# Optimization experiments

Measured on AMD Instinct MI355X. Metric: run time of the kernel, lower is better.

## Reference

```python
import jax, jax.numpy as jnp
import numpy as np
from jax import lax

B, H, W = 2, 256, 256
K = 7
K2 = K * K
IN_CH = 32 * 2 + 81  # 145


def _conv(x, w, b):
    y = lax.conv_general_dilated(x, w, (1, 1), 'SAME', dimension_numbers=('NCHW', 'OIHW', 'NCHW'))
    return y + b[None, :, None, None]


def _lrelu(x):
    return jnp.where(x >= 0, x, 0.1 * x)


def _predictor(x, w1, b1, w2, b2, w3, b3, wo, bo, ww, bw):
    f = _lrelu(_conv(x, w1, b1))
    f = _lrelu(_conv(f, w2, b2))
    f = _lrelu(_conv(f, w3, b3))
    offsets = _conv(f, wo, bo)                     # (B, 2*K2, H, W)
    weights = jax.nn.softmax(_conv(f, ww, bw), 1)  # (B, K2, H, W)
    return offsets, weights


def _sample(image, offsets, weights):
    b, c, h, w = image.shape
    k2 = weights.shape[1]
    off = offsets.reshape(b, k2, 2, h, w)
    dx, dy = off[:, :, 0], off[:, :, 1]
    gy, gx = jnp.meshgrid(jnp.arange(h, dtype=image.dtype), jnp.arange(w, dtype=image.dtype), indexing='ij')
    sx = gx[None, None] + dx  # (b,k2,h,w)
    sy = gy[None, None] + dy
    # Original normalizes with 2*s/(n-1)-1 (align_corners=True formula) but calls
    # grid_sample(align_corners=False): pixel coord = ((g+1)*n - 1)/2 = s*n/(n-1) - 0.5.
    # padding_mode='border' == clamp coord to [0, n-1] before bilinear.
    px = jnp.clip(sx * (w / (w - 1.0)) - 0.5, 0.0, w - 1.0)
    py = jnp.clip(sy * (h / (h - 1.0)) - 0.5, 0.0, h - 1.0)
    x0 = jnp.floor(px)
    y0 = jnp.floor(py)
    fx = (px - x0)[:, None]  # (b,1,k2,h,w)
    fy = (py - y0)[:, None]
    x0i = x0.astype(jnp.int32)
    y0i = y0.astype(jnp.int32)
    x1i = jnp.minimum(x0i + 1, w - 1)
    y1i = jnp.minimum(y0i + 1, h - 1)
    img = image.reshape(b, c, h * w)

    def gather(yi, xi):
        idx = (yi * w + xi).reshape(b, 1, k2 * h * w)
        return jnp.take_along_axis(img, idx, axis=2).reshape(b, c, k2, h, w)

    v00 = gather(y0i, x0i)
    v01 = gather(y0i, x1i)
    v10 = gather(y1i, x0i)
    v11 = gather(y1i, x1i)
    sampled = (v00 * (1 - fx) * (1 - fy) + v01 * fx * (1 - fy)
               + v10 * (1 - fx) * fy + v11 * fx * fy)
    return jnp.einsum('bkhw,bckhw->bchw', weights, sampled)


def setup_inputs() -> dict:
    key = jax.random.key(0)
    ks = iter(jax.random.split(key, 64))

    def nrm(shape, s=1.0):
        return jax.random.normal(next(ks), shape, jnp.float32) * s

    off0 = np.array([[j - K // 2, i - K // 2] for i in range(K) for j in range(K)],
                    np.float32).reshape(-1)  # interleaved (dx, dy) default grid

    def pred_params(p):
        return {
            p + '_w1': nrm((256, IN_CH, 3, 3), 0.02), p + '_b1': jnp.zeros((256,), jnp.float32),
            p + '_w2': nrm((256, 256, 3, 3), 0.02), p + '_b2': jnp.zeros((256,), jnp.float32),
            p + '_w3': nrm((128, 256, 3, 3), 0.02), p + '_b3': jnp.zeros((128,), jnp.float32),
            p + '_wo': nrm((2 * K2, 128, 3, 3), 0.01), p + '_bo': jnp.asarray(off0),
            p + '_ww': nrm((K2, 128, 3, 3), 0.02), p + '_bw': jnp.full((K2,), 1.0 / K2, jnp.float32),
        }

    inp = {
        'frame1': nrm((B, 3, H, W)),
        'frame2': nrm((B, 3, H, W)),
        'feat1': nrm((B, 32, H, W)),
        'feat2': nrm((B, 32, H, W)),
        'corr': nrm((B, 81, H, W)),
    }
    inp.update(pred_params('k1'))
    inp.update(pred_params('k2'))
    inp['bl_w1'] = nrm((64, IN_CH, 3, 3), 0.02)
    inp['bl_b1'] = jnp.zeros((64,), jnp.float32)
    inp['bl_w2'] = nrm((1, 64, 3, 3), 0.02)
    inp['bl_b2'] = jnp.zeros((1,), jnp.float32)
    return inp


def reference(frame1, frame2, feat1, feat2, corr,
              k1_w1, k1_b1, k1_w2, k1_b2, k1_w3, k1_b3, k1_wo, k1_bo, k1_ww, k1_bw,
              k2_w1, k2_b1, k2_w2, k2_b2, k2_w3, k2_b3, k2_wo, k2_bo, k2_ww, k2_bw,
              bl_w1, bl_b1, bl_w2, bl_b2):
    combined = jnp.concatenate([feat1, feat2, corr], axis=1)  # (B,145,H,W)
    off1, wt1 = _predictor(combined, k1_w1, k1_b1, k1_w2, k1_b2, k1_w3, k1_b3, k1_wo, k1_bo, k1_ww, k1_bw)
    off2, wt2 = _predictor(combined, k2_w1, k2_b1, k2_w2, k2_b2, k2_w3, k2_b3, k2_wo, k2_bo, k2_ww, k2_bw)
    s1 = _sample(frame1, off1, wt1)
    s2 = _sample(frame2, off2, wt2)
    blend = jax.nn.sigmoid(_conv(_lrelu(_conv(combined, bl_w1, bl_b1)), bl_w2, bl_b2))
    output = blend * s1 + (1.0 - blend) * s2
    return (output, blend, off1, off2, wt1, wt2)
```

## Files before the change

kernel.cpp:

```cpp
#include <hip/hip_runtime.h>


static constexpr int HW  = 65536;
static constexpr int WID = 256;
static constexpr int PAD = 66564;

using f32x16 = __attribute__((ext_vector_type(16))) float;
using f32x4  = __attribute__((ext_vector_type(4))) float;
using s16x8  = __attribute__((ext_vector_type(8))) short;

__device__ __forceinline__ unsigned short f2b(float f) {
    unsigned u = __builtin_bit_cast(unsigned, f);
    u += 0x7fffu + ((u >> 16) & 1u);
    return (unsigned short)(u >> 16);
}
__device__ __forceinline__ float b2f(unsigned short h) {
    unsigned u = ((unsigned)h) << 16;
    return __builtin_bit_cast(float, u);
}

template <int N> __device__ __forceinline__ void vm_wait() {
    asm volatile("s_waitcnt vmcnt(%0)" :: "n"(N) : "memory");
}

__global__ void pack_x(const float* __restrict__ feat1, const float* __restrict__ feat2,
                       const float* __restrict__ corr, unsigned short* __restrict__ Xc) {
    int idx = blockIdx.x * 256 + threadIdx.x;
    int g  = idx >> 17;
    int bp = idx & (2 * HW - 1);
    int b  = bp >> 16, p = bp & 65535;
    unsigned short v[8];
#pragma unroll
    for (int j = 0; j < 8; ++j) {
        int c = g * 8 + j;
        float val = 0.f;
        if (c < 32)       val = feat1[(size_t)(b * 32 + c) * HW + p];
        else if (c < 64)  val = feat2[(size_t)(b * 32 + (c - 32)) * HW + p];
        else if (c < 145) val = corr [(size_t)(b * 81 + (c - 64)) * HW + p];
        v[j] = f2b(val);
    }
    uint4 u;
    u.x = v[0] | ((unsigned)v[1] << 16);
    u.y = v[2] | ((unsigned)v[3] << 16);
    u.z = v[4] | ((unsigned)v[5] << 16);
    u.w = v[6] | ((unsigned)v[7] << 16);
    int y = p >> 8, x = p & 255;
    size_t cell = (size_t)b * PAD + (size_t)(y + 1) * 258 + (x + 1);
    *reinterpret_cast<uint4*>(Xc + cell * 160 + g * 8) = u;
}

__global__ void pack_w(const float* __restrict__ W, unsigned short* __restrict__ Wp,
                       int OC, int IC, int OCP, int KC) {
    int idx = blockIdx.x * 256 + threadIdx.x;
    int total = 9 * KC * 4 * OCP * 8;
    if (idx >= total) return;
    int i8 = idx & 7;  int r = idx >> 3;
    int oc = r % OCP;  r /= OCP;
    int g  = r & 3;    r >>= 2;
    int kb = r % KC;   int s = r / KC;
    int ic = kb * 32 + g * 8 + i8;
    float v = (oc < OC && ic < IC) ? W[((size_t)(oc * IC + ic)) * 9 + s] : 0.f;
    Wp[idx] = f2b(v);
}

__global__ void zero_border(unsigned short* __restrict__ buf, int C) {
    int idx = blockIdx.x * 256 + threadIdx.x;
    int G = C >> 3;
    int total = 2 * 1028 * G;
    if (idx >= total) return;
    int gi = idx % G; int r = idx / G;
    int ci = r % 1028; int b = r / 1028;
    int row, col;
    if (ci < 258)      { row = 0;            col = ci; }
    else if (ci < 516) { row = 257;          col = ci - 258; }
    else if (ci < 772) { row = ci - 516 + 1; col = 0; }
    else               { row = ci - 772 + 1; col = 257; }
    *reinterpret_cast<uint4*>(buf + ((size_t)b * PAD + row * 258 + col) * C + gi * 8) =
        make_uint4(0u, 0u, 0u, 0u);
}

template <int ICP, int OCF, int OCT, int MODE>
__global__ __launch_bounds__(512, 2) void conv3x3(
    const unsigned short* __restrict__ X,
    const uint4* __restrict__ Wp,
    const float* __restrict__ bias,
    unsigned short* __restrict__ outB,
    float* __restrict__ outF)
{
    constexpr int KC = ICP / 32;
    __shared__ uint4 lds[8192];

    const int t = threadIdx.x;
    const int lane = t & 63, wn = t >> 6;
    const int l31 = lane & 31, hi = lane >> 5;
    const int ocOff = blockIdx.y * 128;

    const int bid = blockIdx.x;
    const int q8  = gridDim.x >> 3;
    const int work = (bid & 7) * q8 + (bid >> 3);
    const int bb = work >> 7;
    const int tt = work & 127;
    const int tr = tt >> 3, tc = tt & 7;

    auto stage_x = [&](int kb2, int slot) {
#pragma unroll
        for (int it = 0; it < 5; ++it) {
            int G = it * 512 + t;
            int g = G / 640;
            int cell = G - g * 640;
            cell = min(cell, 611);
            int rr = cell / 34, cc = cell - rr * 34;
            const unsigned short* src = X +
                ((size_t)bb * PAD + (size_t)(tr * 16 + rr) * 258 + tc * 32 + cc) * ICP +
                kb2 * 32 + g * 8;
            __builtin_amdgcn_global_load_lds(
                (const __attribute__((address_space(1))) unsigned int*)src,
                (__attribute__((address_space(3))) unsigned int*)&lds[slot * 2560 + it * 512 + (t & ~63)],
                16, 0, 0);
        }
    };
    auto stage_wg = [&](int kb2, int dy2, int wslot) {
#pragma unroll
        for (int j = 0; j < 3; ++j) {
            int s = dy2 * 3 + j;
            const uint4* src = Wp + ((size_t)(s * KC + kb2) * 4 + (t >> 7)) * OCF + ocOff + (t & 127);
            __builtin_amdgcn_global_load_lds(
                (const __attribute__((address_space(1))) unsigned int*)src,
                (__attribute__((address_space(3))) unsigned int*)&lds[5120 + wslot * 1536 + j * 512 + (t & ~63)],
                16, 0, 0);
        }
    };

    f32x16 acc[4][2] = {};

    stage_x(0, 0);
    stage_wg(0, 0, 0);

#pragma unroll 1
    for (int kb = 0; kb < KC; ++kb) {
        const int xb = (kb & 1) * 2560;
#pragma unroll
        for (int dy = 0; dy < 3; ++dy) {
            const int wb = 5120 + ((kb * 3 + dy) & 1) * 1536;
            __builtin_amdgcn_s_barrier();
            const bool lastG = (kb == KC - 1) && (dy == 2);
            if (dy == 0) {
                stage_wg(kb, 1, (kb * 3 + 1) & 1);
            } else if (dy == 1) {
                stage_wg(kb, 2, (kb * 3 + 2) & 1);
            } else if (kb + 1 < KC) {
                stage_wg(kb + 1, 0, (3 * (kb + 1)) & 1);
                stage_x(kb + 1, (kb + 1) & 1);
            }
            if (lastG)        vm_wait<0>();
            else if (dy == 2) vm_wait<8>();
            else              vm_wait<3>();

#pragma unroll
            for (int dxi = 0; dxi < 3; ++dxi) {
                uint4 a[2][4], bq[2][2];
#pragma unroll
                for (int ks = 0; ks < 2; ++ks) {
#pragma unroll
                    for (int fm = 0; fm < 4; ++fm)
                        a[ks][fm] = lds[wb + dxi * 512 + (ks * 2 + hi) * 128 + fm * 32 + l31];
#pragma unroll
                    for (int fn = 0; fn < 2; ++fn)
                        bq[ks][fn] = lds[xb + (ks * 2 + hi) * 640 + (wn * 2 + fn + dy) * 34 + dxi + l31];
                }
                __builtin_amdgcn_s_setprio(1);
#pragma unroll
                for (int ks = 0; ks < 2; ++ks)
#pragma unroll
                    for (int fm = 0; fm < 4; ++fm)
#pragma unroll
                        for (int fn = 0; fn < 2; ++fn)
                            acc[fm][fn] = __builtin_amdgcn_mfma_f32_32x32x16_bf16(
                                __builtin_bit_cast(s16x8, a[ks][fm]),
                                __builtin_bit_cast(s16x8, bq[ks][fn]),
                                acc[fm][fn], 0, 0, 0);
                __builtin_amdgcn_s_setprio(0);
            }
        }
    }

#pragma unroll
    for (int fm = 0; fm < 4; ++fm) {
#pragma unroll
        for (int fn = 0; fn < 2; ++fn) {
            const int prow = wn * 2 + fn;
            if (MODE == 0) {
                const size_t cellp = (size_t)bb * PAD + (size_t)(tr * 16 + prow + 1) * 258 + tc * 32 + l31 + 1;
#pragma unroll
                for (int qd = 0; qd < 4; ++qd) {
                    const int goc = ocOff + fm * 32 + qd * 8 + hi * 4;
                    if (goc < OCT) {
                        float4 bv = *reinterpret_cast<const float4*>(bias + goc);
                        const float* bvp = reinterpret_cast<const float*>(&bv);
                        unsigned short o[4];
#pragma unroll
                        for (int j = 0; j < 4; ++j) {
                            float r = acc[fm][fn][qd * 4 + j] + bvp[j];
                            r = (r >= 0.f) ? r : 0.1f * r;
                            o[j] = f2b(r);
                        }
                        uint2 pk;
                        pk.x = o[0] | ((unsigned)o[1] << 16);
                        pk.y = o[2] | ((unsigned)o[3] << 16);
                        *reinterpret_cast<uint2*>(outB + cellp * OCT + goc) = pk;
                    }
                }
            } else {
                const int py = tr * 16 + prow, px = tc * 32 + l31;
#pragma unroll
                for (int qd = 0; qd < 4; ++qd) {
#pragma unroll
                    for (int j = 0; j < 4; ++j) {
                        const int oc = ocOff + fm * 32 + qd * 8 + hi * 4 + j;
                        if (oc < OCT)
                            outF[((size_t)bb * OCT + oc) * HW + py * WID + px] =
                                acc[fm][fn][qd * 4 + j] + bias[oc];
                    }
                }
            }
        }
    }
}

__global__ void softmax49(float* __restrict__ L) {
    int idx = blockIdx.x * 256 + threadIdx.x;
    int b = idx >> 16, p = idx & 65535;
    float* lp = L + (size_t)b * 49 * HW + p;
    float v[49];
    float mx = -1e30f;
#pragma unroll
    for (int k = 0; k < 49; ++k) { v[k] = lp[(size_t)k * HW]; mx = fmaxf(mx, v[k]); }
    float sum = 0.f;
#pragma unroll
    for (int k = 0; k < 49; ++k) { v[k] = expf(v[k] - mx); sum += v[k]; }
    float inv = 1.f / sum;
#pragma unroll
    for (int k = 0; k < 49; ++k) lp[(size_t)k * HW] = v[k] * inv;
}

__global__ void blend2k(const unsigned short* __restrict__ Fb, const float* __restrict__ W2,
                        const float* __restrict__ B2, float* __restrict__ blendOut) {
    int idx = blockIdx.x * 256 + threadIdx.x;
    int b = idx >> 16, p = idx & 65535, y = p >> 8, x = p & 255;
    float acc = B2[0];
#pragma unroll
    for (int ry = 0; ry < 3; ++ry) {
#pragma unroll
        for (int rx = 0; rx < 3; ++rx) {
            const unsigned short* fp = Fb + ((size_t)b * PAD + (size_t)(y + ry) * 258 + (x + rx)) * 64;
#pragma unroll
            for (int g = 0; g < 8; ++g) {
                uint4 u = *reinterpret_cast<const uint4*>(fp + g * 8);
                unsigned w[4] = {u.x, u.y, u.z, u.w};
#pragma unroll
                for (int h = 0; h < 4; ++h) {
                    int c = g * 8 + h * 2;
                    acc += b2f((unsigned short)(w[h] & 0xffffu)) * W2[(c)     * 9 + ry * 3 + rx];
                    acc += b2f((unsigned short)(w[h] >> 16))     * W2[(c + 1) * 9 + ry * 3 + rx];
                }
            }
        }
    }
    blendOut[idx] = 1.f / (1.f + expf(-acc));
}

__global__ void pack_frames(const float* __restrict__ f1, const float* __restrict__ f2,
                            f32x4* __restrict__ Ff) {
    int idx = blockIdx.x * 256 + threadIdx.x;
    int fr = idx >> 17; int bp = idx & (2 * HW - 1);
    const float* src = fr ? f2 : f1;
    int b = bp >> 16, p = bp & 65535;
    f32x4 v;
    v[0] = src[(size_t)(b * 3 + 0) * HW + p];
    v[1] = src[(size_t)(b * 3 + 1) * HW + p];
    v[2] = src[(size_t)(b * 3 + 2) * HW + p];
    v[3] = 0.f;
    Ff[(size_t)fr * 2 * HW + bp] = v;
}

__device__ __forceinline__ void sample_accum4(const f32x4* __restrict__ img,
                                              const float* __restrict__ off,
                                              const float* __restrict__ wt,
                                              int x, int y, f32x4& s) {
    for (int k = 0; k < 49; ++k) {
        float dx = off[(size_t)(2 * k) * HW];
        float dy = off[(size_t)(2 * k + 1) * HW];
        float w  = wt [(size_t)k * HW];
        float px = ((float)x + dx) * (256.f / 255.f) - 0.5f;
        float py = ((float)y + dy) * (256.f / 255.f) - 0.5f;
        px = fminf(fmaxf(px, 0.f), 255.f);
        py = fminf(fmaxf(py, 0.f), 255.f);
        float x0f = floorf(px), y0f = floorf(py);
        float fx = px - x0f, fy = py - y0f;
        int x0 = (int)x0f, y0 = (int)y0f;
        int x1 = min(x0 + 1, 255), y1 = min(y0 + 1, 255);
        const f32x4* r0 = img + y0 * WID;
        const f32x4* r1 = img + y1 * WID;
        f32x4 v = (1.f - fy) * ((1.f - fx) * r0[x0] + fx * r0[x1]) +
                  fy         * ((1.f - fx) * r1[x0] + fx * r1[x1]);
        s += w * v;
    }
}

__global__ void sample_final(const f32x4* __restrict__ Ff,
                             const float* __restrict__ off1, const float* __restrict__ off2,
                             const float* __restrict__ wt1, const float* __restrict__ wt2,
                             const float* __restrict__ blend, float* __restrict__ out) {
    int idx = blockIdx.x * 256 + threadIdx.x;
    int b = idx >> 16, p = idx & 65535, y = p >> 8, x = p & 255;
    f32x4 s1 = {0.f, 0.f, 0.f, 0.f}, s2 = {0.f, 0.f, 0.f, 0.f};
    sample_accum4(Ff + (size_t)b * HW, off1 + (size_t)b * 98 * HW + p,
                  wt1 + (size_t)b * 49 * HW + p, x, y, s1);
    sample_accum4(Ff + (size_t)(2 + b) * HW, off2 + (size_t)b * 98 * HW + p,
                  wt2 + (size_t)b * 49 * HW + p, x, y, s2);
    float bl = blend[idx];
#pragma unroll
    for (int c = 0; c < 3; ++c)
        out[(size_t)(b * 3 + c) * HW + p] = bl * s1[c] + (1.f - bl) * s2[c];
}

extern "C" void kernel_launch(void* const* d_in, const int* in_sizes, int n_in,
                              void* d_out, int out_size, void* d_ws, size_t ws_size,
                              hipStream_t stream) {
    (void)in_sizes; (void)n_in; (void)out_size; (void)ws_size;
    const float* frame1 = (const float*)d_in[0];
    const float* frame2 = (const float*)d_in[1];
    const float* feat1  = (const float*)d_in[2];
    const float* feat2  = (const float*)d_in[3];
    const float* corr   = (const float*)d_in[4];
    const float* Wsrc[2][5];
    const float* Bsrc[2][5];
    for (int pdx = 0; pdx < 2; ++pdx) {
        int base = 5 + pdx * 10;
        for (int l = 0; l < 5; ++l) {
            Wsrc[pdx][l] = (const float*)d_in[base + 2 * l];
            Bsrc[pdx][l] = (const float*)d_in[base + 2 * l + 1];
        }
    }
    const float* bl_w1 = (const float*)d_in[25];
    const float* bl_b1 = (const float*)d_in[26];
    const float* bl_w2 = (const float*)d_in[27];
    const float* bl_b2 = (const float*)d_in[28];

    float* out      = (float*)d_out;
    float* out_bl   = out + 393216;
    float* out_off[2] = {out + 524288,   out + 13369344};
    float* out_wt [2] = {out + 26214400, out + 32636928};

    char* ws = (char*)d_ws;
    size_t o = 0;
    auto alloc = [&](size_t bytes) { char* p = ws + o; o += (bytes + 255) & ~(size_t)255; return p; };
    unsigned short* Xc   = (unsigned short*)alloc((size_t)2 * PAD * 160 * 2);
    unsigned short* bufA = (unsigned short*)alloc((size_t)2 * PAD * 256 * 2);
    unsigned short* bufB = (unsigned short*)alloc((size_t)2 * PAD * 256 * 2);
    unsigned short *WpC1[2], *WpC2[2], *WpC3[2], *WpCo[2], *WpCw[2];
    for (int pdx = 0; pdx < 2; ++pdx) {
        WpC1[pdx] = (unsigned short*)alloc((size_t)9 * 256 * 160 * 2);
        WpC2[pdx] = (unsigned short*)alloc((size_t)9 * 256 * 256 * 2);
        WpC3[pdx] = (unsigned short*)alloc((size_t)9 * 128 * 256 * 2);
        WpCo[pdx] = (unsigned short*)alloc((size_t)9 * 128 * 128 * 2);
        WpCw[pdx] = (unsigned short*)alloc((size_t)9 * 128 * 128 * 2);
    }
    unsigned short* WpBl = (unsigned short*)alloc((size_t)9 * 128 * 160 * 2);
    f32x4* Ff = (f32x4*)bufA;

    auto packw = [&](const float* W, unsigned short* Wp, int OC, int IC, int OCP, int ICP) {
        int total = 9 * OCP * ICP;
        pack_w<<<(total + 255) / 256, 256, 0, stream>>>(W, Wp, OC, IC, OCP, ICP / 32);
    };
    auto zb = [&](unsigned short* buf, int C) {
        int total = 2 * 1028 * (C / 8);
        zero_border<<<(total + 255) / 256, 256, 0, stream>>>(buf, C);
    };

    zb(Xc, 160);
    pack_x<<<(2 * HW * 20) / 256, 256, 0, stream>>>(feat1, feat2, corr, Xc);
    for (int pdx = 0; pdx < 2; ++pdx) {
        packw(Wsrc[pdx][0], WpC1[pdx], 256, 145, 256, 160);
        packw(Wsrc[pdx][1], WpC2[pdx], 256, 256, 256, 256);
        packw(Wsrc[pdx][2], WpC3[pdx], 128, 256, 128, 256);
        packw(Wsrc[pdx][3], WpCo[pdx],  98, 128, 128, 128);
        packw(Wsrc[pdx][4], WpCw[pdx],  49, 128, 128, 128);
    }
    packw(bl_w1, WpBl, 64, 145, 128, 160);
    zb(bufB, 256);

    for (int pdx = 0; pdx < 2; ++pdx) {
        zb(bufA, 256);
        conv3x3<160, 256, 256, 0><<<dim3(256, 2), 512, 0, stream>>>(
            Xc, (const uint4*)WpC1[pdx], Bsrc[pdx][0], bufA, nullptr);
        conv3x3<256, 256, 256, 0><<<dim3(256, 2), 512, 0, stream>>>(
            bufA, (const uint4*)WpC2[pdx], Bsrc[pdx][1], bufB, nullptr);
        zb(bufA, 128);
        conv3x3<256, 128, 128, 0><<<dim3(256, 1), 512, 0, stream>>>(
            bufB, (const uint4*)WpC3[pdx], Bsrc[pdx][2], bufA, nullptr);
        conv3x3<128, 128, 98, 1><<<dim3(256, 1), 512, 0, stream>>>(
            bufA, (const uint4*)WpCo[pdx], Bsrc[pdx][3], nullptr, out_off[pdx]);
        conv3x3<128, 128, 49, 1><<<dim3(256, 1), 512, 0, stream>>>(
            bufA, (const uint4*)WpCw[pdx], Bsrc[pdx][4], nullptr, out_wt[pdx]);
        softmax49<<<512, 256, 0, stream>>>(out_wt[pdx]);
    }

    zb(bufB, 64);
    conv3x3<160, 128, 64, 0><<<dim3(256, 1), 512, 0, stream>>>(
        Xc, (const uint4*)WpBl, bl_b1, bufB, nullptr);
    blend2k<<<512, 256, 0, stream>>>(bufB, bl_w2, bl_b2, out_bl);

    pack_frames<<<(4 * HW) / 256, 256, 0, stream>>>(frame1, frame2, Ff);
    sample_final<<<512, 256, 0, stream>>>(Ff, out_off[0], out_off[1],
                                          out_wt[0], out_wt[1], out_bl, out);
}
```

Before: 1.190 ms.

## Halve conv3x3 block to 4 waves with larger per-wave tiles and software-pipelined LDS reads

Drops the conv3x3 block from 512 to 256 threads. Each wave now computes 4 output rows by 4 output-channel fragments (16 accumulators instead of 8), and staging loops are doubled to cover the same tile. LDS fragment loads are interleaved with MFMA batches in a ping-pong pattern so reads overlap compute. The aim is more reuse of each A/B fragment per LDS read and fewer LDS reads overall. In exchange register pressure rises sharply (256 accumulator floats per lane), and with launch_bounds(256,1) only 4 waves fit per CU, which may expose latency.

```diff
diff --git a/kernel.cpp b/kernel.cpp
--- a/kernel.cpp
+++ b/kernel.cpp
@@ -80,7 +80,7 @@
 }
 
 template <int ICP, int OCF, int OCT, int MODE>
-__global__ __launch_bounds__(512, 2) void conv3x3(
+__global__ __launch_bounds__(256, 1) void conv3x3(
     const unsigned short* __restrict__ X,
     const uint4* __restrict__ Wp,
     const float* __restrict__ bias,
@@ -104,8 +104,8 @@
 
     auto stage_x = [&](int kb2, int slot) {
 #pragma unroll
-        for (int it = 0; it < 5; ++it) {
-            int G = it * 512 + t;
+        for (int it = 0; it < 10; ++it) {
+            int G = it * 256 + t;
             int g = G / 640;
             int cell = G - g * 640;
             cell = min(cell, 611);
@@ -115,7 +115,7 @@
                 kb2 * 32 + g * 8;
             __builtin_amdgcn_global_load_lds(
                 (const __attribute__((address_space(1))) unsigned int*)src,
-                (__attribute__((address_space(3))) unsigned int*)&lds[slot * 2560 + it * 512 + (t & ~63)],
+                (__attribute__((address_space(3))) unsigned int*)&lds[slot * 2560 + it * 256 + (t & ~63)],
                 16, 0, 0);
         }
     };
@@ -123,15 +123,40 @@
 #pragma unroll
         for (int j = 0; j < 3; ++j) {
             int s = dy2 * 3 + j;
-            const uint4* src = Wp + ((size_t)(s * KC + kb2) * 4 + (t >> 7)) * OCF + ocOff + (t & 127);
-            __builtin_amdgcn_global_load_lds(
-                (const __attribute__((address_space(1))) unsigned int*)src,
-                (__attribute__((address_space(3))) unsigned int*)&lds[5120 + wslot * 1536 + j * 512 + (t & ~63)],
-                16, 0, 0);
-        }
-    };
-
-    f32x16 acc[4][2] = {};
+#pragma unroll
+            for (int it2 = 0; it2 < 2; ++it2) {
+                int gg = it2 * 2 + (t >> 7);
+                const uint4* src = Wp + ((size_t)(s * KC + kb2) * 4 + gg) * OCF + ocOff + (t & 127);
+                __builtin_amdgcn_global_load_lds(
+                    (const __attribute__((address_space(1))) unsigned int*)src,
+                    (__attribute__((address_space(3))) unsigned int*)&lds[5120 + wslot * 1536 + j * 512 + it2 * 256 + (t & ~63)],
+                    16, 0, 0);
+            }
+        }
+    };
+
+    f32x16 acc[4][4] = {};
+
+    auto ldA = [&](int wb, int dxi, int ks, uint4 (&a)[4]) {
+#pragma unroll
+        for (int fm = 0; fm < 4; ++fm)
+            a[fm] = lds[wb + dxi * 512 + (ks * 2 + hi) * 128 + fm * 32 + l31];
+    };
+    auto ldB = [&](int xb, int dy, int dxi, int ks, uint4 (&b)[4]) {
+#pragma unroll
+        for (int fn = 0; fn < 4; ++fn)
+            b[fn] = lds[xb + (ks * 2 + hi) * 640 + (wn * 4 + fn + dy) * 34 + dxi + l31];
+    };
+    auto mm = [&](const uint4 (&a)[4], const uint4 (&b)[4]) {
+#pragma unroll
+        for (int fm = 0; fm < 4; ++fm)
+#pragma unroll
+            for (int fn = 0; fn < 4; ++fn)
+                acc[fm][fn] = __builtin_amdgcn_mfma_f32_32x32x16_bf16(
+                    __builtin_bit_cast(s16x8, a[fm]),
+                    __builtin_bit_cast(s16x8, b[fn]),
+                    acc[fm][fn], 0, 0, 0);
+    };
 
     stage_x(0, 0);
     stage_wg(0, 0, 0);
@@ -153,42 +178,30 @@
                 stage_x(kb + 1, (kb + 1) & 1);
             }
             if (lastG)        vm_wait<0>();
-            else if (dy == 2) vm_wait<8>();
-            else              vm_wait<3>();
-
-#pragma unroll
-            for (int dxi = 0; dxi < 3; ++dxi) {
-                uint4 a[2][4], bq[2][2];
-#pragma unroll
-                for (int ks = 0; ks < 2; ++ks) {
-#pragma unroll
-                    for (int fm = 0; fm < 4; ++fm)
-                        a[ks][fm] = lds[wb + dxi * 512 + (ks * 2 + hi) * 128 + fm * 32 + l31];
-#pragma unroll
-                    for (int fn = 0; fn < 2; ++fn)
-                        bq[ks][fn] = lds[xb + (ks * 2 + hi) * 640 + (wn * 2 + fn + dy) * 34 + dxi + l31];
-                }
-                __builtin_amdgcn_s_setprio(1);
-#pragma unroll
-                for (int ks = 0; ks < 2; ++ks)
-#pragma unroll
-                    for (int fm = 0; fm < 4; ++fm)
-#pragma unroll
-                        for (int fn = 0; fn < 2; ++fn)
-                            acc[fm][fn] = __builtin_amdgcn_mfma_f32_32x32x16_bf16(
-                                __builtin_bit_cast(s16x8, a[ks][fm]),
-                                __builtin_bit_cast(s16x8, bq[ks][fn]),
-                                acc[fm][fn], 0, 0, 0);
-                __builtin_amdgcn_s_setprio(0);
-            }
+            else if (dy == 2) vm_wait<16>();
+            else              vm_wait<6>();
+
+            uint4 aE[4], bE[4], aO[4], bO[4];
+            ldA(wb, 0, 0, aE); ldB(xb, dy, 0, 0, bE);
+            ldA(wb, 0, 1, aO); ldB(xb, dy, 0, 1, bO);
+            mm(aE, bE);
+            ldA(wb, 1, 0, aE); ldB(xb, dy, 1, 0, bE);
+            mm(aO, bO);
+            ldA(wb, 1, 1, aO); ldB(xb, dy, 1, 1, bO);
+            mm(aE, bE);
+            ldA(wb, 2, 0, aE); ldB(xb, dy, 2, 0, bE);
+            mm(aO, bO);
+            ldA(wb, 2, 1, aO); ldB(xb, dy, 2, 1, bO);
+            mm(aE, bE);
+            mm(aO, bO);
         }
     }
 
 #pragma unroll
     for (int fm = 0; fm < 4; ++fm) {
 #pragma unroll
-        for (int fn = 0; fn < 2; ++fn) {
-            const int prow = wn * 2 + fn;
+        for (int fn = 0; fn < 4; ++fn) {
+            const int prow = wn * 4 + fn;
             if (MODE == 0) {
                 const size_t cellp = (size_t)bb * PAD + (size_t)(tr * 16 + prow + 1) * 258 + tc * 32 + l31 + 1;
 #pragma unroll
@@ -392,22 +405,22 @@
 
     for (int pdx = 0; pdx < 2; ++pdx) {
         zb(bufA, 256);
-        conv3x3<160, 256, 256, 0><<<dim3(256, 2), 512, 0, stream>>>(
+        conv3x3<160, 256, 256, 0><<<dim3(256, 2), 256, 0, stream>>>(
             Xc, (const uint4*)WpC1[pdx], Bsrc[pdx][0], bufA, nullptr);
-        conv3x3<256, 256, 256, 0><<<dim3(256, 2), 512, 0, stream>>>(
+        conv3x3<256, 256, 256, 0><<<dim3(256, 2), 256, 0, stream>>>(
             bufA, (const uint4*)WpC2[pdx], Bsrc[pdx][1], bufB, nullptr);
         zb(bufA, 128);
-        conv3x3<256, 128, 128, 0><<<dim3(256, 1), 512, 0, stream>>>(
+        conv3x3<256, 128, 128, 0><<<dim3(256, 1), 256, 0, stream>>>(
             bufB, (const uint4*)WpC3[pdx], Bsrc[pdx][2], bufA, nullptr);
-        conv3x3<128, 128, 98, 1><<<dim3(256, 1), 512, 0, stream>>>(
+        conv3x3<128, 128, 98, 1><<<dim3(256, 1), 256, 0, stream>>>(
             bufA, (const uint4*)WpCo[pdx], Bsrc[pdx][3], nullptr, out_off[pdx]);
-        conv3x3<128, 128, 49, 1><<<dim3(256, 1), 512, 0, stream>>>(
+        conv3x3<128, 128, 49, 1><<<dim3(256, 1), 256, 0, stream>>>(
             bufA, (const uint4*)WpCw[pdx], Bsrc[pdx][4], nullptr, out_wt[pdx]);
         softmax49<<<512, 256, 0, stream>>>(out_wt[pdx]);
     }
 
     zb(bufB, 64);
-    conv3x3<160, 128, 64, 0><<<dim3(256, 1), 512, 0, stream>>>(
+    conv3x3<160, 128, 64, 0><<<dim3(256, 1), 256, 0, stream>>>(
         Xc, (const uint4*)WpBl, bl_b1, bufB, nullptr);
     blend2k<<<512, 256, 0, stream>>>(bufB, bl_w2, bl_b2, out_bl);
 
```

Measured after the change: 1.409 ms. 18.4% more time.

## Software-pipeline LDS fragment loads with MFMA and precompute 32-bit load offsets

Applied to the files above, without the earlier changes.

Restructures the conv3x3 inner loop so LDS fragment loads for the next k-step are issued while MFMAs on the previous fragments run, using ping-pong register buffers. Global-to-LDS source addresses are precomputed once as 32-bit byte offsets and incremented per channel block instead of recomputed with 64-bit math. The vmcnt waits are retuned to match the new issue order. The intent is less address arithmetic and hidden LDS latency, at the cost of more live registers and 32-bit offsets that must not overflow.

```diff
diff --git a/kernel.cpp b/kernel.cpp
--- a/kernel.cpp
+++ b/kernel.cpp
@@ -88,6 +88,7 @@
     float* __restrict__ outF)
 {
     constexpr int KC = ICP / 32;
+    constexpr unsigned WSTR = (unsigned)OCF * 64u;
     __shared__ uint4 lds[8192];
 
     const int t = threadIdx.x;
@@ -102,85 +103,104 @@
     const int tt = work & 127;
     const int tr = tt >> 3, tc = tt & 7;
 
-    auto stage_x = [&](int kb2, int slot) {
-#pragma unroll
-        for (int it = 0; it < 5; ++it) {
-            int G = it * 512 + t;
-            int g = G / 640;
-            int cell = G - g * 640;
-            cell = min(cell, 611);
-            int rr = cell / 34, cc = cell - rr * 34;
-            const unsigned short* src = X +
-                ((size_t)bb * PAD + (size_t)(tr * 16 + rr) * 258 + tc * 32 + cc) * ICP +
-                kb2 * 32 + g * 8;
-            __builtin_amdgcn_global_load_lds(
-                (const __attribute__((address_space(1))) unsigned int*)src,
-                (__attribute__((address_space(3))) unsigned int*)&lds[slot * 2560 + it * 512 + (t & ~63)],
-                16, 0, 0);
-        }
+    unsigned xoff[5];
+#pragma unroll
+    for (int it = 0; it < 5; ++it) {
+        int G = it * 512 + t;
+        int g = G / 640;
+        int cell = G - g * 640;
+        cell = min(cell, 611);
+        int rr = cell / 34, cc = cell - rr * 34;
+        xoff[it] = (unsigned)(((bb * PAD + (tr * 16 + rr) * 258 + tc * 32 + cc) * ICP
+                               + g * 8) * 2);
+    }
+    const unsigned wlane = (unsigned)(((t >> 7) * OCF + ocOff + (t & 127)) * 16);
+    const int tdst = t & ~63;
+
+    auto gload = [&](const char* src, uint4* dst) {
+        __builtin_amdgcn_global_load_lds(
+            (const __attribute__((address_space(1))) unsigned int*)src,
+            (__attribute__((address_space(3))) unsigned int*)dst, 16, 0, 0);
+    };
+    auto stage_x = [&](int slot) {
+#pragma unroll
+        for (int it = 0; it < 5; ++it)
+            gload((const char*)X + xoff[it], &lds[slot * 2560 + it * 512 + tdst]);
     };
     auto stage_wg = [&](int kb2, int dy2, int wslot) {
-#pragma unroll
-        for (int j = 0; j < 3; ++j) {
-            int s = dy2 * 3 + j;
-            const uint4* src = Wp + ((size_t)(s * KC + kb2) * 4 + (t >> 7)) * OCF + ocOff + (t & 127);
-            __builtin_amdgcn_global_load_lds(
-                (const __attribute__((address_space(1))) unsigned int*)src,
-                (__attribute__((address_space(3))) unsigned int*)&lds[5120 + wslot * 1536 + j * 512 + (t & ~63)],
-                16, 0, 0);
-        }
-    };
+        const unsigned wg0 = wlane + (unsigned)(dy2 * 3 * KC + kb2) * WSTR;
+#pragma unroll
+        for (int j = 0; j < 3; ++j)
+            gload((const char*)Wp + wg0 + (unsigned)(j * KC) * WSTR,
+                  &lds[5120 + wslot * 1536 + j * 512 + tdst]);
+    };
+
+    const unsigned aA0 = (unsigned)((hi * 128 + l31) * 16) + 81920u;
+    const unsigned bA0 = (unsigned)((hi * 640 + wn * 68 + l31) * 16);
+    const char* ldsc = (const char*)lds;
 
     f32x16 acc[4][2] = {};
 
-    stage_x(0, 0);
+    auto ldA = [&](unsigned aAg, int dxi, int ks, uint4 (&a)[4]) {
+#pragma unroll
+        for (int fm = 0; fm < 4; ++fm)
+            a[fm] = *(const uint4*)(ldsc + aAg + (unsigned)((dxi * 512 + ks * 256 + fm * 32) * 16));
+    };
+    auto ldB = [&](unsigned bAg, int dy, int dxi, int ks, uint4 (&b)[2]) {
+#pragma unroll
+        for (int fn = 0; fn < 2; ++fn)
+            b[fn] = *(const uint4*)(ldsc + bAg + (unsigned)((ks * 1280 + (fn + dy) * 34 + dxi) * 16));
+    };
+    auto mm = [&](const uint4 (&a)[4], const uint4 (&b)[2]) {
+#pragma unroll
+        for (int fm = 0; fm < 4; ++fm)
+#pragma unroll
+            for (int fn = 0; fn < 2; ++fn)
+                acc[fm][fn] = __builtin_amdgcn_mfma_f32_32x32x16_bf16(
+                    __builtin_bit_cast(s16x8, a[fm]),
+                    __builtin_bit_cast(s16x8, b[fn]),
+                    acc[fm][fn], 0, 0, 0);
+    };
+
+    stage_x(0);
     stage_wg(0, 0, 0);
 
 #pragma unroll 1
     for (int kb = 0; kb < KC; ++kb) {
-        const int xb = (kb & 1) * 2560;
+        const unsigned bAg = bA0 + (unsigned)((kb & 1) * 40960);
 #pragma unroll
         for (int dy = 0; dy < 3; ++dy) {
-            const int wb = 5120 + ((kb * 3 + dy) & 1) * 1536;
+            const unsigned aAg = aA0 + (unsigned)(((kb + dy) & 1) * 24576);
             __builtin_amdgcn_s_barrier();
-            const bool lastG = (kb == KC - 1) && (dy == 2);
             if (dy == 0) {
-                stage_wg(kb, 1, (kb * 3 + 1) & 1);
+                stage_wg(kb, 1, (kb + 1) & 1);
+                vm_wait<6>();
             } else if (dy == 1) {
-                stage_wg(kb, 2, (kb * 3 + 2) & 1);
+                stage_wg(kb, 2, kb & 1);
+                vm_wait<6>();
             } else if (kb + 1 < KC) {
-                stage_wg(kb + 1, 0, (3 * (kb + 1)) & 1);
-                stage_x(kb + 1, (kb + 1) & 1);
+                stage_wg(kb + 1, 0, (kb + 1) & 1);
+#pragma unroll
+                for (int it = 0; it < 5; ++it) xoff[it] += 64u;
+                stage_x((kb + 1) & 1);
+                vm_wait<16>();
+            } else {
+                vm_wait<0>();
             }
-            if (lastG)        vm_wait<0>();
-            else if (dy == 2) vm_wait<8>();
-            else              vm_wait<3>();
-
-#pragma unroll
-            for (int dxi = 0; dxi < 3; ++dxi) {
-                uint4 a[2][4], bq[2][2];
-#pragma unroll
-                for (int ks = 0; ks < 2; ++ks) {
-#pragma unroll
-                    for (int fm = 0; fm < 4; ++fm)
-                        a[ks][fm] = lds[wb + dxi * 512 + (ks * 2 + hi) * 128 + fm * 32 + l31];
-#pragma unroll
-                    for (int fn = 0; fn < 2; ++fn)
-                        bq[ks][fn] = lds[xb + (ks * 2 + hi) * 640 + (wn * 2 + fn + dy) * 34 + dxi + l31];
-                }
-                __builtin_amdgcn_s_setprio(1);
-#pragma unroll
-                for (int ks = 0; ks < 2; ++ks)
-#pragma unroll
-                    for (int fm = 0; fm < 4; ++fm)
-#pragma unroll
-                        for (int fn = 0; fn < 2; ++fn)
-                            acc[fm][fn] = __builtin_amdgcn_mfma_f32_32x32x16_bf16(
-                                __builtin_bit_cast(s16x8, a[ks][fm]),
-                                __builtin_bit_cast(s16x8, bq[ks][fn]),
-                                acc[fm][fn], 0, 0, 0);
-                __builtin_amdgcn_s_setprio(0);
-            }
+
+            uint4 aE[4], aO[4], bE[2], bO[2];
+            ldA(aAg, 0, 0, aE); ldB(bAg, dy, 0, 0, bE);
+            ldA(aAg, 0, 1, aO); ldB(bAg, dy, 0, 1, bO);
+            mm(aE, bE);
+            ldA(aAg, 1, 0, aE); ldB(bAg, dy, 1, 0, bE);
+            mm(aO, bO);
+            ldA(aAg, 1, 1, aO); ldB(bAg, dy, 1, 1, bO);
+            mm(aE, bE);
+            ldA(aAg, 2, 0, aE); ldB(bAg, dy, 2, 0, bE);
+            mm(aO, bO);
+            ldA(aAg, 2, 1, aO); ldB(bAg, dy, 2, 1, bO);
+            mm(aE, bE);
+            mm(aO, bO);
         }
     }
 
```

After: 1.204 ms. About the same (+1.2%).
